# Kernel tuning notes

Measured on AMD Instinct MI355X. Metric: run time of the kernel, lower is better.

## Reference

```python
import jax, jax.numpy as jnp
import numpy as np

K = 9  # 3x3 kernel taps

def _conv3x3(x, w, b):
    # standard 3x3 conv, stride 1, pad 1, NCHW
    y = jax.lax.conv_general_dilated(x, w, (1, 1), [(1, 1), (1, 1)],
                                     dimension_numbers=('NCHW', 'OIHW', 'NCHW'))
    return y + b[None, :, None, None]

def setup_inputs() -> dict:
    key = jax.random.key(0)
    ks = jax.random.split(key, 4)
    B, C, Cout, H, W = 2, 256, 256, 128, 128
    x = jax.random.normal(ks[0], (B, C, H, W), jnp.float32)
    w_off = jax.random.normal(ks[1], (3 * K, C, 3, 3), jnp.float32) * 0.01
    b_off = jnp.zeros((3 * K,), jnp.float32)
    weight = jax.random.normal(ks[2], (Cout, C, 3, 3), jnp.float32) * (1.0 / np.sqrt(K * C))
    bias = jnp.zeros((Cout,), jnp.float32)
    gamma = jnp.ones((Cout,), jnp.float32)
    beta = jnp.zeros((Cout,), jnp.float32)
    return {"x": x, "w_off": w_off, "b_off": b_off, "weight": weight,
            "bias": bias, "gamma": gamma, "beta": beta}

def _deform_gather(x, off_y, off_x, mask):
    # x: [B,C,H,W]; off_y/off_x/mask: [B,K,H,W]
    # returns modulated bilinear samples [B,C,K,H,W]
    B, C, H, W = x.shape
    kh = (jnp.arange(K, dtype=x.dtype) // 3).reshape(1, K, 1, 1)
    kw = (jnp.arange(K, dtype=x.dtype) % 3).reshape(1, K, 1, 1)
    # sampling position per tap: base - pad + tap*dilation + learned offset
    py = jnp.arange(H, dtype=x.dtype).reshape(1, 1, H, 1) - 1.0 + kh + off_y
    px = jnp.arange(W, dtype=x.dtype).reshape(1, 1, 1, W) - 1.0 + kw + off_x
    y0 = jnp.floor(py); x0 = jnp.floor(px)
    wy1 = py - y0; wx1 = px - x0
    xf = x.reshape(B, C, H * W)
    def corner(iy, ix, wgt):
        valid = (iy >= 0) & (iy <= H - 1) & (ix >= 0) & (ix <= W - 1)
        iyc = jnp.clip(iy, 0, H - 1).astype(jnp.int32)
        ixc = jnp.clip(ix, 0, W - 1).astype(jnp.int32)
        lin = (iyc * W + ixc).reshape(B, 1, K * H * W)
        g = jnp.take_along_axis(xf, lin, axis=2).reshape(B, C, K, H, W)
        return g * jnp.where(valid, wgt, 0.0)[:, None]  # zero outside borders
    val = (corner(y0,     x0,     (1 - wy1) * (1 - wx1))
         + corner(y0,     x0 + 1, (1 - wy1) * wx1)
         + corner(y0 + 1, x0,     wy1 * (1 - wx1))
         + corner(y0 + 1, x0 + 1, wy1 * wx1))
    return val * mask[:, None]

def reference(x, w_off, b_off, weight, bias, gamma, beta):
    B, C, H, W = x.shape
    om = _conv3x3(x, w_off, b_off)  # [B, 3K, H, W]
    off_y = om[:, :K]
    off_x = om[:, K:2 * K]
    m = jax.nn.sigmoid(om[:, 2 * K:])  # modulation mask
    sampled = _deform_gather(x, off_y, off_x, m)  # [B,C,K,H,W]
    Cout = weight.shape[0]
    y = jnp.einsum('bckhw,ock->bohw', sampled, weight.reshape(Cout, C, K))
    y = y + bias[None, :, None, None]
    # BatchNorm2d (training-mode batch stats, eps=1e-5) + ReLU
    mu = jnp.mean(y, axis=(0, 2, 3), keepdims=True)
    var = jnp.var(y, axis=(0, 2, 3), keepdims=True)
    yn = (y - mu) * jax.lax.rsqrt(var + 1e-5)
    return jax.nn.relu(yn * gamma[None, :, None, None] + beta[None, :, None, None])
```

## Files before the change

### kernel.cpp

```cpp
#include <hip/hip_runtime.h>
#include <hip/hip_fp16.h>
#include <math.h>

#define HW 16384
#define Cc 256
#define CO 256

typedef unsigned short u16;
typedef unsigned int   u32;
typedef __attribute__((ext_vector_type(8))) _Float16 f16x8;
typedef __attribute__((ext_vector_type(4))) float f32x4;

__device__ __forceinline__ u16 f2h(float f) {
    return __half_as_ushort(__float2half(f));
}

__global__ void k_prep(const float* __restrict__ w, const float* __restrict__ wof,
                       u16* __restrict__ wfr, u16* __restrict__ wofr) {
    int id = blockIdx.x * 256 + threadIdx.x;
    if (id < 589824) {
        int i    = id & 7;
        int lane = (id >> 3) & 63;
        int fb   = id >> 9;
        int k32  = fb % 72;
        int ot   = fb / 72;
        int o  = ot * 16 + (lane & 15);
        int K  = k32 * 32 + (lane >> 4) * 8 + i;
        int kt = K >> 8;
        int c  = K & 255;
        wfr[id] = f2h(w[((size_t)o * 256 + c) * 9 + kt]);
    } else if (id < 663552) {
        int id2  = id - 589824;
        int i    = id2 & 7;
        int lane = (id2 >> 3) & 63;
        int fb   = id2 >> 9;
        int k32  = fb % 72;
        int mt   = fb / 72;
        int o  = mt * 16 + (lane & 15);
        int K  = k32 * 32 + (lane >> 4) * 8 + i;
        int t  = K >> 8;
        int c  = K & 255;
        float v = (o < 27) ? wof[((size_t)o * 256 + c) * 9 + t] : 0.0f;
        wofr[id2] = f2h(v);
    }
}

__global__ __launch_bounds__(256) void k_xt(const float* __restrict__ x, u16* __restrict__ Xt) {
    const int tid = threadIdx.x;
    const int bid = blockIdx.x;
    const int hw0 = (bid & 255) * 64;
    const int b   = bid >> 8;
    const int hwl = tid & 63;
    const int cg  = tid >> 6;
    const int hw  = hw0 + hwl;
    const float* xb = x + ((size_t)b << 22);
    u16* dst = Xt + (((size_t)b << 14) + hw) * 256 + cg * 64;
    #pragma unroll
    for (int oct = 0; oct < 8; ++oct) {
        int c0 = cg * 64 + oct * 8;
        u32 pk[4];
        #pragma unroll
        for (int q = 0; q < 4; ++q) {
            float v0 = xb[((size_t)(c0 + 2 * q) << 14) + hw];
            float v1 = xb[((size_t)(c0 + 2 * q + 1) << 14) + hw];
            pk[q] = (u32)f2h(v0) | ((u32)f2h(v1) << 16);
        }
        *(uint4*)(dst + oct * 8) = make_uint4(pk[0], pk[1], pk[2], pk[3]);
    }
}

__global__ __launch_bounds__(256) void k_offmfma(const u16* __restrict__ Xt,
                                                 const u16* __restrict__ wofr,
                                                 const float* __restrict__ bof,
                                                 float* __restrict__ om) {
    const int tid  = threadIdx.x;
    const int wid  = tid >> 6;
    const int lane = tid & 63;
    const int bid  = blockIdx.x;
    const int wq   = bid & 1;
    const int h    = (bid >> 1) & 127;
    const int b    = bid >> 8;

    const int lr = lane & 15;
    const int lg = lane >> 4;
    const int w  = wq * 64 + wid * 16 + lr;

    f32x4 acc0 = (f32x4)0.0f, acc1 = (f32x4)0.0f;
    const u16* XtB = Xt + (((size_t)b << 14) << 8);

    for (int t = 0; t < 9; ++t) {
        int dh = t / 3 - 1;
        int dw = t % 3 - 1;
        int hh = h + dh;
        int ww = w + dw;
        bool valid = (hh >= 0) && (hh < 128) && (ww >= 0) && (ww < 128);
        int hc = min(max(hh, 0), 127);
        int wc = min(max(ww, 0), 127);
        const u16* xrow = XtB + ((size_t)(hc * 128 + wc) << 8) + lg * 8;
        #pragma unroll
        for (int c32 = 0; c32 < 8; ++c32) {
            int k32 = t * 8 + c32;
            f16x8 bv = *(const f16x8*)(xrow + c32 * 32);
            if (!valid) bv = (f16x8)0;
            f16x8 a0 = *(const f16x8*)(wofr + (((size_t)k32 * 64 + lane) << 3));
            f16x8 a1 = *(const f16x8*)(wofr + ((((size_t)(72 + k32)) * 64 + lane) << 3));
            acc0 = __builtin_amdgcn_mfma_f32_16x16x32_f16(a0, bv, acc0, 0, 0, 0);
            acc1 = __builtin_amdgcn_mfma_f32_16x16x32_f16(a1, bv, acc1, 0, 0, 0);
        }
    }

    float* omb = om + ((size_t)b * 27 << 14) + h * 128 + w;
    #pragma unroll
    for (int j = 0; j < 4; ++j) {
        int o = lg * 4 + j;
        omb[(size_t)o << 14] = acc0[j] + bof[o];
        int o1 = 16 + lg * 4 + j;
        if (o1 < 27) omb[(size_t)o1 << 14] = acc1[j] + bof[o1];
    }
}

__global__ __launch_bounds__(512) void k_sgemm(const u16* __restrict__ Xt,
                                               const float* __restrict__ om,
                                               const u16* __restrict__ wfr,
                                               const float* __restrict__ bias,
                                               float* __restrict__ y,
                                               float* __restrict__ psum) {
    __shared__ int4    soff[9][64];
    __shared__ __half2 swt2[9][64][4];
    __shared__ __align__(16) u16 Blds[2][4096];

    const int tid  = threadIdx.x;
    const int wid  = tid >> 6;
    const int lane = tid & 63;
    const int bid  = ((blockIdx.x & 7) << 6) | (blockIdx.x >> 3);
    const int p0   = bid * 64;
    const int b    = p0 >> 14;
    const int hwb  = p0 & 16383;

    for (int e = tid; e < 576; e += 512) {
        int t = e >> 6, j = e & 63;
        int hw = hwb + j;
        int h = hw >> 7, wc = hw & 127;
        const size_t ob = (size_t)b * 27 * HW;
        float oy = om[ob + (size_t)t * HW + hw];
        float ox = om[ob + (size_t)(9 + t) * HW + hw];
        float mv = om[ob + (size_t)(18 + t) * HW + hw];
        mv = 1.0f / (1.0f + expf(-mv));
        float py = (float)h - 1.0f + (float)(t / 3) + oy;
        float px = (float)wc - 1.0f + (float)(t % 3) + ox;
        float y0f = floorf(py), x0f = floorf(px);
        float wy = py - y0f, wx = px - x0f;
        int iy = (int)y0f, ix = (int)x0f;
        float w4[4] = {(1.0f - wy) * (1.0f - wx), (1.0f - wy) * wx,
                       wy * (1.0f - wx),          wy * wx};
        const int dy[4] = {0, 0, 1, 1};
        const int dx[4] = {0, 1, 0, 1};
        int of[4];
        #pragma unroll
        for (int r = 0; r < 4; ++r) {
            int yy = iy + dy[r], xx = ix + dx[r];
            bool v = (yy >= 0) && (yy <= 127) && (xx >= 0) && (xx <= 127);
            int yc = min(max(yy, 0), 127);
            int xc = min(max(xx, 0), 127);
            of[r] = yc * 128 + xc;
            swt2[t][j][r] = __float2half2_rn(v ? w4[r] * mv : 0.0f);
        }
        soff[t][j] = make_int4(of[0], of[1], of[2], of[3]);
    }
    __syncthreads();

    const int jp    = tid >> 3;
    const int kloc8 = (((tid & 7) ^ (jp & 7)) << 3);
    const u16* XtB  = Xt + (((size_t)b << 14) << 8);

    const int lg = lane >> 4;
    const int lr = lane & 15;

    f32x4 acc[2][4];
    #pragma unroll
    for (int m = 0; m < 2; ++m)
        #pragma unroll
        for (int n = 0; n < 4; ++n) acc[m][n] = (f32x4)0.0f;

    auto gload = [&](int s, uint4* gg) {
        int t = s >> 2;
        int c = ((s & 3) << 6) + kloc8;
        int4 oa = soff[t][jp];
        gg[0] = *(const uint4*)(XtB + (size_t)oa.x * 256 + c);
        gg[1] = *(const uint4*)(XtB + (size_t)oa.y * 256 + c);
        gg[2] = *(const uint4*)(XtB + (size_t)oa.z * 256 + c);
        gg[3] = *(const uint4*)(XtB + (size_t)oa.w * 256 + c);
    };
    auto gcomb = [&](int s, const uint4* gg, int buf) {
        int t = s >> 2;
        __half2 w0 = swt2[t][jp][0];
        __half2 w1 = swt2[t][jp][1];
        __half2 w2 = swt2[t][jp][2];
        __half2 w3 = swt2[t][jp][3];
        const __half2* c0 = (const __half2*)&gg[0];
        const __half2* c1 = (const __half2*)&gg[1];
        const __half2* c2 = (const __half2*)&gg[2];
        const __half2* c3 = (const __half2*)&gg[3];
        u32 o4[4];
        #pragma unroll
        for (int q = 0; q < 4; ++q) {
            __half2 o = __hmul2(c0[q], w0);
            o = __hfma2(c1[q], w1, o);
            o = __hfma2(c2[q], w2, o);
            o = __hfma2(c3[q], w3, o);
            o4[q] = *(const u32*)&o;
        }
        *(uint4*)((char*)&Blds[buf][0] + tid * 16) = make_uint4(o4[0], o4[1], o4[2], o4[3]);
    };
    auto aload = [&](int k32g, f16x8 dst2[2][2]) {
        #pragma unroll
        for (int kk = 0; kk < 2; ++kk)
            #pragma unroll
            for (int m = 0; m < 2; ++m)
                dst2[kk][m] = *(const f16x8*)(wfr +
                    ((size_t)((wid * 2 + m) * 72 + k32g + kk) << 9) + (size_t)lane * 8);
    };

    f16x8 af[2][2];
    {
        uint4 g[4];
        gload(0, g);
        aload(0, af);
        gcomb(0, g, 0);
    }
    __syncthreads();

    int cur = 0;
    for (int s = 0; s < 36; ++s) {
        const int nxt = cur ^ 1;
        uint4 gn[4];
        f16x8 afn[2][2];
        if (s < 35) {
            gload(s + 1, gn);
            aload(2 * (s + 1), afn);
        }

        const char* bb2 = (const char*)&Blds[cur][0];
        #pragma unroll
        for (int kk = 0; kk < 2; ++kk) {
            f16x8 bfv[4];
            #pragma unroll
            for (int n = 0; n < 4; ++n) {
                int row  = n * 16 + lr;
                int boff = row * 128 + ((kk * 64 + lg * 16) ^ ((row & 7) << 4));
                bfv[n] = *(const f16x8*)(bb2 + boff);
            }
            #pragma unroll
            for (int m = 0; m < 2; ++m)
                #pragma unroll
                for (int n = 0; n < 4; ++n)
                    acc[m][n] = __builtin_amdgcn_mfma_f32_16x16x32_f16(af[kk][m], bfv[n], acc[m][n], 0, 0, 0);
        }

        if (s < 35) {
            gcomb(s + 1, gn, nxt);
            #pragma unroll
            for (int kk = 0; kk < 2; ++kk)
                #pragma unroll
                for (int m = 0; m < 2; ++m)
                    af[kk][m] = afn[kk][m];
        }
        __syncthreads();
        cur = nxt;
    }

    const int hw0  = hwb + lr;
    const int slot = (bid & 31) << 9;
    #pragma unroll
    for (int m = 0; m < 2; ++m) {
        #pragma unroll
        for (int jj = 0; jj < 4; ++jj) {
            int o = wid * 32 + m * 16 + lg * 4 + jj;
            float bv = bias[o];
            float* ya = y + ((size_t)b * 256 + o) * HW + hw0;
            float ssum = 0.0f, ssq = 0.0f;
            #pragma unroll
            for (int n = 0; n < 4; ++n) {
                float v = acc[m][n][jj] + bv;
                ya[n * 16] = v;
                ssum += v;
                ssq  += v * v;
            }
            #pragma unroll
            for (int d = 1; d < 16; d <<= 1) {
                ssum += __shfl_xor(ssum, d);
                ssq  += __shfl_xor(ssq, d);
            }
            if (lr == 0) {
                atomicAdd(&psum[slot + o], ssum);
                atomicAdd(&psum[slot + 256 + o], ssq);
            }
        }
    }
}

__global__ void k_stats2(const float* __restrict__ psum, float* __restrict__ st) {
    int o = threadIdx.x;
    float s = 0.0f, q = 0.0f;
    #pragma unroll 8
    for (int r = 0; r < 32; ++r) {
        s += psum[(r << 9) + o];
        q += psum[(r << 9) + 256 + o];
    }
    float mu  = s / 32768.0f;
    float var = q / 32768.0f - mu * mu;
    st[o]       = mu;
    st[256 + o] = rsqrtf(var + 1e-5f);
}

__global__ void k_norm(const float* __restrict__ y, const float* __restrict__ stats,
                       const float* __restrict__ gamma, const float* __restrict__ beta,
                       float* __restrict__ out) {
    int i4 = blockIdx.x * 256 + threadIdx.x;
    if (i4 >= (2 * CO * HW) / 4) return;
    int o = (i4 >> 12) & 255;
    float g  = gamma[o] * stats[256 + o];
    float bt = beta[o] - stats[o] * g;
    float4 v = ((const float4*)y)[i4];
    float4 r;
    r.x = fmaxf(fmaf(v.x, g, bt), 0.0f);
    r.y = fmaxf(fmaf(v.y, g, bt), 0.0f);
    r.z = fmaxf(fmaf(v.z, g, bt), 0.0f);
    r.w = fmaxf(fmaf(v.w, g, bt), 0.0f);
    ((float4*)out)[i4] = r;
}

extern "C" void kernel_launch(void* const* d_in, const int* in_sizes, int n_in,
                              void* d_out, int out_size, void* d_ws, size_t ws_size,
                              hipStream_t stream) {
    const float* x      = (const float*)d_in[0];
    const float* w_off  = (const float*)d_in[1];
    const float* b_off  = (const float*)d_in[2];
    const float* weight = (const float*)d_in[3];
    const float* bias   = (const float*)d_in[4];
    const float* gamma  = (const float*)d_in[5];
    const float* beta   = (const float*)d_in[6];
    float* out = (float*)d_out;

    float* ws   = (float*)d_ws;
    float* om   = ws;
    float* st   = om + 884736;
    float* ps   = st + 512;
    float* yb   = ps + 16384;
    u16*   wfr  = (u16*)(yb + 8388608);
    u16*   wofr = wfr + 589824;
    u16*   Xt   = wofr + 73728;

    k_prep<<<2592, 256, 0, stream>>>(weight, w_off, wfr, wofr);
    k_xt<<<512, 256, 0, stream>>>(x, Xt);
    hipMemsetAsync(ps, 0, 16384 * sizeof(float), stream);
    k_offmfma<<<512, 256, 0, stream>>>(Xt, wofr, b_off, om);

    k_sgemm<<<512, 512, 0, stream>>>(Xt, om, wfr, bias, yb, ps);

    k_stats2<<<1, 256, 0, stream>>>(ps, st);
    k_norm<<<(2 * CO * HW / 4 + 255) / 256, 256, 0, stream>>>(yb, st, gamma, beta, out);
}
```

Measured before the change: 123.8 us.

## Store conv output as fp16, unroll pipeline by two, precompute byte offsets, raise MFMA priority

The pre-norm activation buffer is now stored as fp16 instead of fp32, which halves the write traffic in the GEMM epilogue and the read traffic in the normalize kernel. The batch statistics still come from fp32 values. The main loop is manually unrolled by two with ping-pong A-fragment registers, avoiding register copies. Gather offsets are precomputed as byte offsets with 32-bit address arithmetic, and s_setprio is raised around the MFMA block. fp16 storage of y adds rounding error before normalization.

Result: slower. 143.2 us (+15.7%).

```diff
diff --git a/kernel.cpp b/kernel.cpp
--- a/kernel.cpp
+++ b/kernel.cpp
@@ -123,7 +123,7 @@
                                                const float* __restrict__ om,
                                                const u16* __restrict__ wfr,
                                                const float* __restrict__ bias,
-                                               float* __restrict__ y,
+                                               u16* __restrict__ y,
                                                float* __restrict__ psum) {
     __shared__ int4    soff[9][64];
     __shared__ __half2 swt2[9][64][4];
@@ -162,7 +162,7 @@
             bool v = (yy >= 0) && (yy <= 127) && (xx >= 0) && (xx <= 127);
             int yc = min(max(yy, 0), 127);
             int xc = min(max(xx, 0), 127);
-            of[r] = yc * 128 + xc;
+            of[r] = (yc * 128 + xc) << 9;
             swt2[t][j][r] = __float2half2_rn(v ? w4[r] * mv : 0.0f);
         }
         soff[t][j] = make_int4(of[0], of[1], of[2], of[3]);
@@ -170,8 +170,8 @@
     __syncthreads();
 
     const int jp    = tid >> 3;
-    const int kloc8 = (((tid & 7) ^ (jp & 7)) << 3);
-    const u16* XtB  = Xt + (((size_t)b << 14) << 8);
+    const int kbyte = (((tid & 7) ^ (jp & 7)) << 4);
+    const char* XtC = (const char*)(Xt + (((size_t)b << 14) << 8));
 
     const int lg = lane >> 4;
     const int lr = lane & 15;
@@ -183,13 +183,12 @@
         for (int n = 0; n < 4; ++n) acc[m][n] = (f32x4)0.0f;
 
     auto gload = [&](int s, uint4* gg) {
-        int t = s >> 2;
-        int c = ((s & 3) << 6) + kloc8;
-        int4 oa = soff[t][jp];
-        gg[0] = *(const uint4*)(XtB + (size_t)oa.x * 256 + c);
-        gg[1] = *(const uint4*)(XtB + (size_t)oa.y * 256 + c);
-        gg[2] = *(const uint4*)(XtB + (size_t)oa.z * 256 + c);
-        gg[3] = *(const uint4*)(XtB + (size_t)oa.w * 256 + c);
+        int cb = ((s & 3) << 7) + kbyte;
+        int4 oa = soff[s >> 2][jp];
+        gg[0] = *(const uint4*)(XtC + (u32)(oa.x + cb));
+        gg[1] = *(const uint4*)(XtC + (u32)(oa.y + cb));
+        gg[2] = *(const uint4*)(XtC + (u32)(oa.z + cb));
+        gg[3] = *(const uint4*)(XtC + (u32)(oa.w + cb));
     };
     auto gcomb = [&](int s, const uint4* gg, int buf) {
         int t = s >> 2;
@@ -220,27 +219,9 @@
                 dst2[kk][m] = *(const f16x8*)(wfr +
                     ((size_t)((wid * 2 + m) * 72 + k32g + kk) << 9) + (size_t)lane * 8);
     };
-
-    f16x8 af[2][2];
-    {
-        uint4 g[4];
-        gload(0, g);
-        aload(0, af);
-        gcomb(0, g, 0);
-    }
-    __syncthreads();
-
-    int cur = 0;
-    for (int s = 0; s < 36; ++s) {
-        const int nxt = cur ^ 1;
-        uint4 gn[4];
-        f16x8 afn[2][2];
-        if (s < 35) {
-            gload(s + 1, gn);
-            aload(2 * (s + 1), afn);
-        }
-
+    auto domfma = [&](int cur, f16x8 afv[2][2]) {
         const char* bb2 = (const char*)&Blds[cur][0];
+        __builtin_amdgcn_s_setprio(1);
         #pragma unroll
         for (int kk = 0; kk < 2; ++kk) {
             f16x8 bfv[4];
@@ -254,19 +235,47 @@
             for (int m = 0; m < 2; ++m)
                 #pragma unroll
                 for (int n = 0; n < 4; ++n)
-                    acc[m][n] = __builtin_amdgcn_mfma_f32_16x16x32_f16(af[kk][m], bfv[n], acc[m][n], 0, 0, 0);
-        }
-
-        if (s < 35) {
-            gcomb(s + 1, gn, nxt);
-            #pragma unroll
-            for (int kk = 0; kk < 2; ++kk)
-                #pragma unroll
-                for (int m = 0; m < 2; ++m)
-                    af[kk][m] = afn[kk][m];
-        }
-        __syncthreads();
-        cur = nxt;
+                    acc[m][n] = __builtin_amdgcn_mfma_f32_16x16x32_f16(afv[kk][m], bfv[n], acc[m][n], 0, 0, 0);
+        }
+        __builtin_amdgcn_s_setprio(0);
+    };
+
+    f16x8 afA[2][2], afB[2][2];
+    {
+        uint4 g[4];
+        gload(0, g);
+        aload(0, afA);
+        gcomb(0, g, 0);
+    }
+    __syncthreads();
+
+    int cur = 0;
+    #pragma unroll 1
+    for (int sp = 0; sp < 18; ++sp) {
+        const int s0 = 2 * sp;
+        const int s1 = s0 + 1;
+        {
+            uint4 gn[4];
+            gload(s0 + 1, gn);
+            aload(2 * (s0 + 1), afB);
+            domfma(cur, afA);
+            gcomb(s0 + 1, gn, cur ^ 1);
+            __syncthreads();
+            cur ^= 1;
+        }
+        {
+            uint4 gn[4];
+            if (s1 < 35) {
+                gload(s1 + 1, gn);
+                aload(2 * (s1 + 1), afA);
+            }
+            domfma(cur, afB);
+            if (s1 < 35) {
+                gcomb(s1 + 1, gn, cur ^ 1);
+            }
+            __syncthreads();
+            cur ^= 1;
+        }
     }
 
     const int hw0  = hwb + lr;
@@ -277,12 +286,12 @@
         for (int jj = 0; jj < 4; ++jj) {
             int o = wid * 32 + m * 16 + lg * 4 + jj;
             float bv = bias[o];
-            float* ya = y + ((size_t)b * 256 + o) * HW + hw0;
+            u16* ya = y + ((size_t)b * 256 + o) * HW + hw0;
             float ssum = 0.0f, ssq = 0.0f;
             #pragma unroll
             for (int n = 0; n < 4; ++n) {
                 float v = acc[m][n][jj] + bv;
-                ya[n * 16] = v;
+                ya[n * 16] = f2h(v);
                 ssum += v;
                 ssq  += v * v;
             }
@@ -313,21 +322,32 @@
     st[256 + o] = rsqrtf(var + 1e-5f);
 }
 
-__global__ void k_norm(const float* __restrict__ y, const float* __restrict__ stats,
+__global__ void k_norm(const u16* __restrict__ y, const float* __restrict__ stats,
                        const float* __restrict__ gamma, const float* __restrict__ beta,
                        float* __restrict__ out) {
-    int i4 = blockIdx.x * 256 + threadIdx.x;
-    if (i4 >= (2 * CO * HW) / 4) return;
-    int o = (i4 >> 12) & 255;
+    int i8 = blockIdx.x * 256 + threadIdx.x;
+    if (i8 >= (2 * CO * HW) / 8) return;
+    int o = ((i8 * 8) >> 14) & 255;
     float g  = gamma[o] * stats[256 + o];
     float bt = beta[o] - stats[o] * g;
-    float4 v = ((const float4*)y)[i4];
-    float4 r;
-    r.x = fmaxf(fmaf(v.x, g, bt), 0.0f);
-    r.y = fmaxf(fmaf(v.y, g, bt), 0.0f);
-    r.z = fmaxf(fmaf(v.z, g, bt), 0.0f);
-    r.w = fmaxf(fmaf(v.w, g, bt), 0.0f);
-    ((float4*)out)[i4] = r;
+    uint4 v = ((const uint4*)y)[i8];
+    const __half2* h2 = (const __half2*)&v;
+    float4 r0, r1;
+    float2 f0 = __half22float2(h2[0]);
+    float2 f1 = __half22float2(h2[1]);
+    float2 f2 = __half22float2(h2[2]);
+    float2 f3 = __half22float2(h2[3]);
+    r0.x = fmaxf(fmaf(f0.x, g, bt), 0.0f);
+    r0.y = fmaxf(fmaf(f0.y, g, bt), 0.0f);
+    r0.z = fmaxf(fmaf(f1.x, g, bt), 0.0f);
+    r0.w = fmaxf(fmaf(f1.y, g, bt), 0.0f);
+    r1.x = fmaxf(fmaf(f2.x, g, bt), 0.0f);
+    r1.y = fmaxf(fmaf(f2.y, g, bt), 0.0f);
+    r1.z = fmaxf(fmaf(f3.x, g, bt), 0.0f);
+    r1.w = fmaxf(fmaf(f3.y, g, bt), 0.0f);
+    float4* op = (float4*)(out + (size_t)i8 * 8);
+    op[0] = r0;
+    op[1] = r1;
 }
 
 extern "C" void kernel_launch(void* const* d_in, const int* in_sizes, int n_in,
@@ -346,8 +366,8 @@
     float* om   = ws;
     float* st   = om + 884736;
     float* ps   = st + 512;
-    float* yb   = ps + 16384;
-    u16*   wfr  = (u16*)(yb + 8388608);
+    u16*   yb   = (u16*)(ps + 16384);
+    u16*   wfr  = yb + 8388608;
     u16*   wofr = wfr + 589824;
     u16*   Xt   = wofr + 73728;
 
@@ -359,5 +379,5 @@
     k_sgemm<<<512, 512, 0, stream>>>(Xt, om, wfr, bias, yb, ps);
 
     k_stats2<<<1, 256, 0, stream>>>(ps, st);
-    k_norm<<<(2 * CO * HW / 4 + 255) / 256, 256, 0, stream>>>(yb, st, gamma, beta, out);
-}
+    k_norm<<<(2 * CO * HW / 8 + 255) / 256, 256, 0, stream>>>(yb, st, gamma, beta, out);
+}
```
